# Optimization experiments

Measured on AMD Instinct MI355X. Metric: run time of the kernel, lower is better.

## Reference

```python
import jax, jax.numpy as jnp
import numpy as np

B, C, L, M, EMB, HID = 32, 64, 8192, 32, 256, 64

def setup_inputs() -> dict:
    key = jax.random.key(0)
    ks = jax.random.split(key, 14)
    s_w = 1.0 / (C * C)
    s_a = 1.0 / EMB
    return {
        "x": jax.random.normal(ks[0], (B, C, L), jnp.float32),
        "emb": jax.random.normal(ks[1], (B, EMB), jnp.float32),
        "weights_pos": s_w * jax.random.normal(ks[2], (C, C, M, 2), jnp.float32),
        "weights_neg": s_w * jax.random.normal(ks[3], (C, C, M, 2), jnp.float32),
        "A_real_pos": s_a * jax.random.normal(ks[4], (M, EMB), jnp.float32),
        "A_imag_pos": s_a * jax.random.normal(ks[5], (M, EMB), jnp.float32),
        "A_real_neg": s_a * jax.random.normal(ks[6], (M, EMB), jnp.float32),
        "A_imag_neg": s_a * jax.random.normal(ks[7], (M, EMB), jnp.float32),
        "tm_w1": 0.05 * jax.random.normal(ks[8], (HID, EMB), jnp.float32),
        "tm_b1": jnp.zeros((HID,), jnp.float32),
        "tm_w2": 0.05 * jax.random.normal(ks[9], (2 * C, HID), jnp.float32),
        "tm_b2": jnp.zeros((2 * C,), jnp.float32),
        "lin_w": 0.05 * jax.random.normal(ks[10], (C, C), jnp.float32),
        "lin_b": jnp.zeros((C,), jnp.float32),
    }

def reference(x, emb, weights_pos, weights_neg, A_real_pos, A_imag_pos,
              A_real_neg, A_imag_neg, tm_w1, tm_b1, tm_w2, tm_b2, lin_w, lin_b):
    b, c, l = x.shape
    m = weights_pos.shape[2]
    k = l // 2 + 1
    # ---- SpectralConv1d branch ----
    x_ft = jnp.fft.rfft(x, norm="ortho")  # [B,C,K] complex
    wp = weights_pos[..., 0] + 1j * weights_pos[..., 1]  # [Ci,Co,M]
    wn = weights_neg[..., 0] + 1j * weights_neg[..., 1]
    phi_p = (emb @ A_real_pos.T) + 1j * (emb @ A_imag_pos.T)  # [B,M]
    phi_n = (emb @ A_real_neg.T) + 1j * (emb @ A_imag_neg.T)
    out_pos = jnp.einsum("bim,iom->bom", x_ft[:, :, :m], wp) * phi_p[:, None, :]
    out_neg = jnp.einsum("bim,iom->bom", x_ft[:, :, k - m:], wn) * phi_n[:, None, :]
    out_ft = jnp.zeros((b, c, k), dtype=x_ft.dtype)
    out_ft = out_ft.at[:, :, :m].set(out_pos).at[:, :, k - m:].set(out_neg)
    x1 = jnp.fft.irfft(out_ft, n=l, norm="ortho")  # [B,C,L]
    # ---- Conv1DTime branch (FiLM-style) ----
    h = jax.nn.silu(emb @ tm_w1.T + tm_b1)          # [B,HID]
    gb = h @ tm_w2.T + tm_b2                         # [B,2C]
    gamma, beta = gb[:, :c], gb[:, c:]
    xl = jnp.einsum("bcl,oc->bol", x, lin_w) + lin_b[None, :, None]
    x2 = xl * (1.0 + gamma[:, :, None]) + beta[:, :, None]
    return jax.nn.silu(x1 + x2)
```

## Files before the change

kernel.cpp:

```cpp
#include <hip/hip_runtime.h>
#include <math.h>

#define L_ 8192
#define EMB_ 256
#define HID_ 64

typedef __attribute__((ext_vector_type(8))) short bf16x8;
typedef __attribute__((ext_vector_type(4))) float f32x4;
typedef __attribute__((ext_vector_type(4))) int i32x4;

#define OFF_TFB  0
#define OFF_TLB  262144
#define OFF_AFB  524288
#define OFF_XFRP 917504
#define OFF_B2   3014656
#define OFF_PHI  3016704
#define OFF_GB   3020800

__device__ inline int pkbf(float a, float b) {
    int r;
    asm volatile("v_cvt_pk_bf16_f32 %0, %1, %2" : "=v"(r) : "v"(a), "v"(b));
    return r;
}
__device__ inline bf16x8 asbf(i32x4 v) { union { i32x4 i; bf16x8 h; } u; u.i = v; return u.h; }
#define MFMA(A,B,C) __builtin_amdgcn_mfma_f32_16x16x32_bf16((A),(B),(C),0,0,0)

__device__ inline ushort f2bf(float v) {
    unsigned b = __float_as_uint(v);
    return (ushort)((b + 0x7FFFu + ((b >> 16) & 1u)) >> 16);
}
__device__ inline float bf2f(ushort h) { return __uint_as_float(((unsigned)h) << 16); }
__device__ inline float hwsin(float rev) { float r; asm("v_sin_f32 %0, %1" : "=v"(r) : "v"(rev)); return r; }
__device__ inline float hwcos(float rev) { float r; asm("v_cos_f32 %0, %1" : "=v"(r) : "v"(rev)); return r; }

__global__ __launch_bounds__(256) void k_init(ushort* __restrict__ TLB, ushort* __restrict__ TFB,
        const float* __restrict__ emb,
        const float* __restrict__ Arp, const float* __restrict__ Aip,
        const float* __restrict__ Arn, const float* __restrict__ Ain, float* __restrict__ phi,
        const float* __restrict__ w1, const float* __restrict__ b1,
        const float* __restrict__ w2, const float* __restrict__ b2, float* __restrict__ gb) {
    int bid = blockIdx.x;
    if (bid < 4096) {
        int idx = bid * 256 + threadIdx.x;
        int f, l; ushort* dst;
        if (idx < 524288) {
            int u = idx;
            int e = u & 7, lane = (u >> 3) & 63, ct = (u >> 9) & 3, kstep = u >> 11;
            l = kstep * 32 + ((lane >> 4) << 3) + e;
            f = ct * 16 + (lane & 15);
            dst = TLB + u;
        } else {
            int u = idx - 524288;
            int e = u & 7, lane = (u >> 3) & 63, ts = (u >> 9) & 1, lt = u >> 10;
            l = lt * 16 + (lane & 15);
            f = ts * 32 + ((lane >> 4) << 3) + e;
            dst = TFB + u;
        }
        int fr = f & 31; bool sinp = (f & 32) != 0;
        int r = (fr * l) & (L_ - 1);
        float rev = (float)r * (1.0f / (float)L_);
        float v = sinp ? hwsin(rev) : hwcos(rev);
        *dst = f2bf(v);
    } else if (bid < 4112) {
        int tid = (bid - 4096) * 256 + threadIdx.x;
        int b = tid >> 7;
        int mm = (tid >> 2) & 31;
        int cmp = tid & 3;
        const float* A = (cmp == 0) ? Arp : (cmp == 1) ? Aip : (cmp == 2) ? Arn : Ain;
        const float4* e4 = (const float4*)(emb + b * EMB_);
        const float4* a4 = (const float4*)(A + mm * EMB_);
        float acc = 0.f;
        for (int q = 0; q < EMB_ / 4; ++q) {
            float4 ev = e4[q], av = a4[q];
            acc += ev.x * av.x + ev.y * av.y + ev.z * av.z + ev.w * av.w;
        }
        phi[tid] = acc;
    } else {
        __shared__ float h[HID_];
        int b = bid - 4112, t = threadIdx.x;
        if (t < HID_) {
            const float4* e4 = (const float4*)(emb + b * EMB_);
            const float4* w4 = (const float4*)(w1 + t * EMB_);
            float acc = b1[t];
            for (int q = 0; q < EMB_ / 4; ++q) {
                float4 ev = e4[q], wv = w4[q];
                acc += ev.x * wv.x + ev.y * wv.y + ev.z * wv.z + ev.w * wv.w;
            }
            h[t] = acc / (1.f + expf(-acc));
        }
        __syncthreads();
        if (t < 128) {
            float g = b2[t];
            const float4* h4 = (const float4*)h;
            const float4* w4 = (const float4*)(w2 + t * HID_);
            for (int q = 0; q < HID_ / 4; ++q) {
                float4 hv = h4[q], wv = w4[q];
                g += hv.x * wv.x + hv.y * wv.y + hv.z * wv.z + hv.w * wv.w;
            }
            if (t < 64) gb[(b * 64 + t) * 2 + 0] = 1.f + g;
            else        gb[(b * 64 + (t - 64)) * 2 + 1] = g;
        }
    }
}

__global__ __launch_bounds__(256) void k_dft(const float* __restrict__ x,
        const ushort* __restrict__ TLB, float* __restrict__ xfrp) {
    __shared__ float sP[4][16][132];
    int stripe = blockIdx.x >> 3;
    int lseg = blockIdx.x & 7;
    int w = threadIdx.x >> 6;
    int lane = threadIdx.x & 63;
    int row = lane & 15, koff = (lane >> 4) << 3;
    int r0 = stripe * 16;
    int kb0 = lseg * 1024 + w * 256;

    f32x4 acc[8];
    #pragma unroll
    for (int i = 0; i < 8; ++i) acc[i] = (f32x4){0.f, 0.f, 0.f, 0.f};

    const float* ap = x + (size_t)(r0 + row) * L_ + kb0 + koff;
    const i32x4* tb = (const i32x4*)TLB;
    int tbase = (kb0 >> 5) * 256 + lane;
    const i32x4 SM = {(int)0x80000000, (int)0x80000000, (int)0x80000000, (int)0x80000000};

    float4 xa0 = *(const float4*)(ap);
    float4 xc0 = *(const float4*)(ap + 4);
    float4 xa1 = *(const float4*)(ap + 32);
    float4 xc1 = *(const float4*)(ap + 36);
    float4 xa2 = *(const float4*)(ap + 64);
    float4 xc2 = *(const float4*)(ap + 68);
    i32x4 t0 = tb[tbase], t1 = tb[tbase + 64], t2 = tb[tbase + 128], t3 = tb[tbase + 192];
    #pragma unroll
    for (int ks = 0; ks < 8; ++ks) {
        float4 nxa = {0,0,0,0}, nxc = {0,0,0,0};
        i32x4 n0 = t0, n1 = t1, n2 = t2, n3 = t3;
        if (ks < 5) {
            nxa = *(const float4*)(ap + (ks + 3) * 32);
            nxc = *(const float4*)(ap + (ks + 3) * 32 + 4);
        }
        if (ks < 7) {
            int ti = tbase + (ks + 1) * 256;
            n0 = tb[ti]; n1 = tb[ti + 64]; n2 = tb[ti + 128]; n3 = tb[ti + 192];
        }
        int h0 = pkbf(xa0.x, xa0.y), h1 = pkbf(xa0.z, xa0.w);
        int h2 = pkbf(xc0.x, xc0.y), h3 = pkbf(xc0.z, xc0.w);
        bf16x8 AH = asbf((i32x4){h0, h1, h2, h3});
        acc[0] = MFMA(AH, asbf(t0), acc[0]); acc[4] = MFMA(AH, asbf(t0 ^ SM), acc[4]);
        acc[1] = MFMA(AH, asbf(t1), acc[1]); acc[5] = MFMA(AH, asbf(t1 ^ SM), acc[5]);
        acc[2] = MFMA(AH, asbf(t2), acc[2]); acc[6] = MFMA(AH, asbf(t2 ^ SM), acc[6]);
        acc[3] = MFMA(AH, asbf(t3), acc[3]); acc[7] = MFMA(AH, asbf(t3 ^ SM), acc[7]);
        xa0 = xa1; xc0 = xc1; xa1 = xa2; xc1 = xc2; xa2 = nxa; xc2 = nxc;
        t0 = n0; t1 = n1; t2 = n2; t3 = n3;
    }
    int crow = (lane >> 4) << 2;
    int ccol = lane & 15;
    #pragma unroll
    for (int ct = 0; ct < 8; ++ct)
        #pragma unroll
        for (int r = 0; r < 4; ++r)
            sP[w][crow + r][ct * 16 + ccol] = acc[ct][r];
    __syncthreads();
    #pragma unroll
    for (int i = 0; i < 8; ++i) {
        int e = threadIdx.x + 256 * i;
        int rr = e & 15, cc = e >> 4;
        float s = sP[0][rr][cc] + sP[1][rr][cc] + sP[2][rr][cc] + sP[3][rr][cc];
        xfrp[((size_t)(lseg * 128 + cc)) * 2048 + r0 + rr] = s;
    }
}

__global__ __launch_bounds__(256) void k_mix(const float* __restrict__ xfrt,
        const float* __restrict__ wpos, const float* __restrict__ wneg,
        const float* __restrict__ phi, const float* __restrict__ lw,
        const float* __restrict__ lb, const float* __restrict__ gb,
        ushort* __restrict__ afb, float* __restrict__ bias2) {
    int bi = blockIdx.x;
    int tid = threadIdx.x;
    if (bi >= 256) {
        int b = bi - 256;
        ushort* dst = afb + (size_t)b * 24576;
        #pragma unroll
        for (int j = 0; j < 16; ++j) {
            int u = tid + 256 * j;
            int e = u & 7, lane = (u >> 3) & 63, mt = (u >> 9) & 3, ks2 = u >> 11;
            int c = mt * 16 + (lane & 15);
            int kk = ((lane >> 4) << 3) + e;
            float v = lw[c * 64 + ks2 * 32 + kk] * gb[(b * 64 + c) * 2];
            ushort hi = f2bf(v);
            int base = (((4 + ks2) * 4 + mt) * 64 + lane) * 16;
            dst[base + e] = hi;
            dst[base + 8 + e] = f2bf(v - bf2f(hi));
        }
        if (tid < 64) {
            float g1 = gb[(b * 64 + tid) * 2], be = gb[(b * 64 + tid) * 2 + 1];
            bias2[b * 64 + tid] = lb[tid] * g1 + be;
        }
        return;
    }
    __shared__ float sW[64][64][2];
    __shared__ float sXr[8][64], sXi[8][64];
    int bh = bi & 3, side = (bi >> 2) & 1, mm = bi >> 3;
    int slot = side ? (31 - mm) : mm;
    int colR = side ? (64 + slot) : mm;
    int colI = side ? (96 + slot) : (32 + mm);

    const float* W = side ? wneg : wpos;
    #pragma unroll
    for (int j = 0; j < 16; ++j) {
        int fidx = tid + 256 * j;
        int i = fidx >> 6, o = fidx & 63;
        float2 wv = *(const float2*)&W[(size_t)(i * 64 + o) * 64 + mm * 2];
        sW[i][o][0] = wv.x;
        sW[i][o][1] = wv.y;
    }
    {
        const float2* pR = (const float2*)(xfrt + (size_t)colR * 2048 + bh * 512);
        const float2* pI = (const float2*)(xfrt + (size_t)colI * 2048 + bh * 512);
        float2 aR = {0, 0}, aI = {0, 0};
        #pragma unroll
        for (int s = 0; s < 8; ++s) {
            float2 vR = pR[(size_t)s * 131072 + tid];
            float2 vI = pI[(size_t)s * 131072 + tid];
            aR.x += vR.x; aR.y += vR.y;
            aI.x += vI.x; aI.y += vI.y;
        }
        if (!side) { aI.x = -aI.x; aI.y = -aI.y; }
        *(float2*)&sXr[tid >> 5][(tid & 31) * 2] = aR;
        *(float2*)&sXi[tid >> 5][(tid & 31) * 2] = aI;
    }
    __syncthreads();

    int o = tid & 63, bg = tid >> 6;
    const float invL = 1.f / (float)L_;
    float fac = (slot == 0) ? invL : 2.f * invL;
    int comp = side ? 2 : 0;
    int e = slot & 7, kgrp = slot >> 3;
    int mt = o >> 4, lane = kgrp * 16 + (o & 15);
    #pragma unroll
    for (int bl = 0; bl < 2; ++bl) {
        int b_local = bg * 2 + bl;
        int b = bh * 8 + b_local;
        float sre = 0.f, sim = 0.f;
        #pragma unroll 16
        for (int i = 0; i < 64; ++i) {
            float wr = sW[i][o][0], wi = sW[i][o][1];
            float xr = sXr[b_local][i], xi = sXi[b_local][i];
            sre += xr * wr - xi * wi;
            sim += xr * wi + xi * wr;
        }
        const float* ph = &phi[(b * 32 + mm) * 4 + (side ? 2 : 0)];
        float phr = ph[0], phim = ph[1];
        float Pre = sre * phr - sim * phim;
        float Pim = sre * phim + sim * phr;
        float a = fac * Pre;
        float bcoef = (slot == 0) ? 0.f : (side ? 2.f * invL * Pim : -2.f * invL * Pim);
        ushort* dst = afb + (size_t)b * 24576;
        ushort hiA = f2bf(a);
        int baseA = ((comp * 4 + mt) * 64 + lane) * 16;
        dst[baseA + e] = hiA;
        dst[baseA + 8 + e] = f2bf(a - bf2f(hiA));
        ushort hiB = f2bf(bcoef);
        int baseB = (((comp + 1) * 4 + mt) * 64 + lane) * 16;
        dst[baseB + e] = hiB;
        dst[baseB + 8 + e] = f2bf(bcoef - bf2f(hiB));
    }
}

#define XISSUE(ts, xv)                                                                   \
    _Pragma("unroll")                                                                    \
    for (int nj = 0; nj < 2; ++nj) {                                                     \
        const float* xp = x + (size_t)(b * 64 + (ts) * 32 + kgrp * 8) * L_               \
                            + lbase + nj * 16 + col;                                     \
        _Pragma("unroll")                                                                \
        for (int e = 0; e < 8; ++e) xv[nj][e] = xp[(size_t)e * L_];                      \
    }

#define TPART(ts)                                                                        \
    {                                                                                    \
        i32x4 bh_[2];                                                                    \
        _Pragma("unroll")                                                                \
        for (int nj = 0; nj < 2; ++nj)                                                   \
            bh_[nj] = tb[((lt0 + nj) * 2 + (ts)) * 64 + lane];                           \
        _Pragma("unroll")                                                                \
        for (int mt = 0; mt < 4; ++mt) {                                                 \
            i32x4 ah0 = ab[(((ts) * 4 + mt) * 64 + lane) * 2];                           \
            i32x4 ah1 = ab[(((2 + (ts)) * 4 + mt) * 64 + lane) * 2];                     \
            bf16x8 AH0 = asbf(ah0), AH1 = asbf(ah1);                                     \
            _Pragma("unroll")                                                            \
            for (int nj = 0; nj < 2; ++nj) {                                             \
                acc[mt][nj] = MFMA(AH0, asbf(bh_[nj]), acc[mt][nj]);                     \
                acc[mt][nj] = MFMA(AH1, asbf(bh_[nj] ^ SM), acc[mt][nj]);                \
            }                                                                            \
        }                                                                                \
    }

#define XPART(ts, xv)                                                                    \
    _Pragma("unroll")                                                                    \
    for (int nj = 0; nj < 2; ++nj) {                                                     \
        int h0 = pkbf(xv[nj][0], xv[nj][1]), h1 = pkbf(xv[nj][2], xv[nj][3]);            \
        int h2 = pkbf(xv[nj][4], xv[nj][5]), h3 = pkbf(xv[nj][6], xv[nj][7]);            \
        bf16x8 XH = asbf((i32x4){h0, h1, h2, h3});                                       \
        _Pragma("unroll")                                                                \
        for (int mt = 0; mt < 4; ++mt) {                                                 \
            i32x4 ah = ab[(((4 + (ts)) * 4 + mt) * 64 + lane) * 2];                      \
            acc[mt][nj] = MFMA(asbf(ah), XH, acc[mt][nj]);                               \
        }                                                                                \
    }

__global__ __launch_bounds__(256, 3) void k_fuse(const float* __restrict__ x,
        const ushort* __restrict__ TFB, const ushort* __restrict__ AFB,
        const float* __restrict__ bias2, float* __restrict__ out) {
    int b = blockIdx.x >> 6, lt = blockIdx.x & 63;
    int w = threadIdx.x >> 6, lane = threadIdx.x & 63;
    int col = lane & 15, kgrp = lane >> 4;
    int lbase = lt * 128 + w * 32;
    int lt0 = lbase >> 4;
    const i32x4* tb = (const i32x4*)TFB;
    const i32x4* ab = (const i32x4*)AFB + (size_t)b * 3072;

    f32x4 acc[4][2];
    #pragma unroll
    for (int i = 0; i < 4; ++i)
        #pragma unroll
        for (int j = 0; j < 2; ++j) acc[i][j] = (f32x4){0.f, 0.f, 0.f, 0.f};

    int sm = (col & 1) ? (int)0x80008000 : 0;
    i32x4 SM = {sm, sm, sm, sm};

    float xva[2][8], xvb[2][8];
    XISSUE(0, xva)
    XISSUE(1, xvb)
    TPART(0)
    XPART(0, xva)
    TPART(1)
    XPART(1, xvb)

    #pragma unroll
    for (int mt = 0; mt < 4; ++mt) {
        #pragma unroll
        for (int r = 0; r < 4; ++r) {
            int c = mt * 16 + kgrp * 4 + r;
            float bias = bias2[b * 64 + c];
            float* op = out + (size_t)(b * 64 + c) * L_ + lbase + col;
            #pragma unroll
            for (int nj = 0; nj < 2; ++nj) {
                float v = acc[mt][nj][r] + bias;
                op[nj * 16] = v / (1.f + __expf(-v));
            }
        }
    }
}

extern "C" void kernel_launch(void* const* d_in, const int* in_sizes, int n_in,
                              void* d_out, int out_size, void* d_ws, size_t ws_size,
                              hipStream_t stream) {
    const float* x    = (const float*)d_in[0];
    const float* emb  = (const float*)d_in[1];
    const float* wpos = (const float*)d_in[2];
    const float* wneg = (const float*)d_in[3];
    const float* Arp  = (const float*)d_in[4];
    const float* Aip  = (const float*)d_in[5];
    const float* Arn  = (const float*)d_in[6];
    const float* Ain  = (const float*)d_in[7];
    const float* w1   = (const float*)d_in[8];
    const float* b1   = (const float*)d_in[9];
    const float* w2   = (const float*)d_in[10];
    const float* b2   = (const float*)d_in[11];
    const float* lw   = (const float*)d_in[12];
    const float* lb   = (const float*)d_in[13];
    float* out = (float*)d_out;
    float* ws = (float*)d_ws;
    ushort* TFB  = (ushort*)(ws + OFF_TFB);
    ushort* TLB  = (ushort*)(ws + OFF_TLB);
    ushort* AFB  = (ushort*)(ws + OFF_AFB);
    float*  XFRP = ws + OFF_XFRP;
    float*  B2   = ws + OFF_B2;
    float*  PHI  = ws + OFF_PHI;
    float*  GB   = ws + OFF_GB;

    hipLaunchKernelGGL(k_init,  dim3(4144), dim3(256), 0, stream,
                       TLB, TFB, emb, Arp, Aip, Arn, Ain, PHI, w1, b1, w2, b2, GB);
    hipLaunchKernelGGL(k_dft,   dim3(1024), dim3(256), 0, stream, x, TLB, XFRP);
    hipLaunchKernelGGL(k_mix,   dim3(288),  dim3(256), 0, stream, XFRP, wpos, wneg, PHI,
                       lw, lb, GB, AFB, B2);
    hipLaunchKernelGGL(k_fuse,  dim3(2048), dim3(256), 0, stream, x, TFB, AFB, B2, out);
}
```

Measured before the change: 69.11 us.

## Emit bf16 transposed x from DFT kernel and pre-transpose spectral weights

The DFT kernel now writes the bf16-packed x values into a channel-interleaved workspace buffer. The fused output kernel reads these with a few 16-byte vector loads instead of 16 strided fp32 loads and reconverting them to bf16. The spectral weights are also transposed once in the init kernel, so the mixing kernel can load them with contiguous float4 reads. This trades extra global writes (scattered 2-byte stores in k_dft) and extra workspace for cheaper, coalesced reads downstream.

```diff
diff --git a/kernel.cpp b/kernel.cpp
--- a/kernel.cpp
+++ b/kernel.cpp
@@ -16,6 +16,8 @@
 #define OFF_B2   3014656
 #define OFF_PHI  3016704
 #define OFF_GB   3020800
+#define OFF_WT   3024896
+#define OFF_XT   3549184
 
 __device__ inline int pkbf(float a, float b) {
     int r;
@@ -38,7 +40,8 @@
         const float* __restrict__ Arp, const float* __restrict__ Aip,
         const float* __restrict__ Arn, const float* __restrict__ Ain, float* __restrict__ phi,
         const float* __restrict__ w1, const float* __restrict__ b1,
-        const float* __restrict__ w2, const float* __restrict__ b2, float* __restrict__ gb) {
+        const float* __restrict__ w2, const float* __restrict__ b2, float* __restrict__ gb,
+        const float* __restrict__ wpos, const float* __restrict__ wneg, float* __restrict__ WT) {
     int bid = blockIdx.x;
     if (bid < 4096) {
         int idx = bid * 256 + threadIdx.x;
@@ -75,7 +78,7 @@
             acc += ev.x * av.x + ev.y * av.y + ev.z * av.z + ev.w * av.w;
         }
         phi[tid] = acc;
-    } else {
+    } else if (bid < 4144) {
         __shared__ float h[HID_];
         int b = bid - 4112, t = threadIdx.x;
         if (t < HID_) {
@@ -100,11 +103,24 @@
             if (t < 64) gb[(b * 64 + t) * 2 + 0] = 1.f + g;
             else        gb[(b * 64 + (t - 64)) * 2 + 1] = g;
         }
+    } else {
+        int t = bid - 4144;
+        int side = t >> 6, i = t & 63;
+        const float* W = side ? wneg : wpos;
+        const float* src = W + (size_t)i * 4096;
+        int tid = threadIdx.x;
+        #pragma unroll
+        for (int j = 0; j < 8; ++j) {
+            int u = tid + 256 * j;
+            int mm = u >> 6, o = u & 63;
+            float2 v = *(const float2*)(src + o * 64 + mm * 2);
+            *(float2*)(WT + ((size_t)(side * 32 + mm)) * 8192 + i * 128 + o * 2) = v;
+        }
     }
 }
 
 __global__ __launch_bounds__(256) void k_dft(const float* __restrict__ x,
-        const ushort* __restrict__ TLB, float* __restrict__ xfrp) {
+        const ushort* __restrict__ TLB, float* __restrict__ xfrp, ushort* __restrict__ XT) {
     __shared__ float sP[4][16][132];
     int stripe = blockIdx.x >> 3;
     int lseg = blockIdx.x & 7;
@@ -145,6 +161,13 @@
         int h0 = pkbf(xa0.x, xa0.y), h1 = pkbf(xa0.z, xa0.w);
         int h2 = pkbf(xc0.x, xc0.y), h3 = pkbf(xc0.z, xc0.w);
         bf16x8 AH = asbf((i32x4){h0, h1, h2, h3});
+        {
+            ushort* xtp = XT + (((size_t)stripe * 8192 + kb0 + koff + ks * 32) << 4) + row;
+            xtp[0]   = (ushort)h0;  xtp[16]  = (ushort)((unsigned)h0 >> 16);
+            xtp[32]  = (ushort)h1;  xtp[48]  = (ushort)((unsigned)h1 >> 16);
+            xtp[64]  = (ushort)h2;  xtp[80]  = (ushort)((unsigned)h2 >> 16);
+            xtp[96]  = (ushort)h3;  xtp[112] = (ushort)((unsigned)h3 >> 16);
+        }
         acc[0] = MFMA(AH, asbf(t0), acc[0]); acc[4] = MFMA(AH, asbf(t0 ^ SM), acc[4]);
         acc[1] = MFMA(AH, asbf(t1), acc[1]); acc[5] = MFMA(AH, asbf(t1 ^ SM), acc[5]);
         acc[2] = MFMA(AH, asbf(t2), acc[2]); acc[6] = MFMA(AH, asbf(t2 ^ SM), acc[6]);
@@ -170,7 +193,7 @@
 }
 
 __global__ __launch_bounds__(256) void k_mix(const float* __restrict__ xfrt,
-        const float* __restrict__ wpos, const float* __restrict__ wneg,
+        const float* __restrict__ WT,
         const float* __restrict__ phi, const float* __restrict__ lw,
         const float* __restrict__ lb, const float* __restrict__ gb,
         ushort* __restrict__ afb, float* __restrict__ bias2) {
@@ -204,14 +227,14 @@
     int colR = side ? (64 + slot) : mm;
     int colI = side ? (96 + slot) : (32 + mm);
 
-    const float* W = side ? wneg : wpos;
-    #pragma unroll
-    for (int j = 0; j < 16; ++j) {
-        int fidx = tid + 256 * j;
-        int i = fidx >> 6, o = fidx & 63;
-        float2 wv = *(const float2*)&W[(size_t)(i * 64 + o) * 64 + mm * 2];
-        sW[i][o][0] = wv.x;
-        sW[i][o][1] = wv.y;
+    {
+        const float4* wt = (const float4*)(WT + ((size_t)(side * 32 + mm)) * 8192);
+        float* sWlin = &sW[0][0][0];
+        #pragma unroll
+        for (int j = 0; j < 8; ++j) {
+            int u = tid + 256 * j;
+            *(float4*)&sWlin[u * 4] = wt[u];
+        }
     }
     {
         const float2* pR = (const float2*)(xfrt + (size_t)colR * 2048 + bh * 512);
@@ -265,15 +288,6 @@
         dst[baseB + 8 + e] = f2bf(bcoef - bf2f(hiB));
     }
 }
-
-#define XISSUE(ts, xv)                                                                   \
-    _Pragma("unroll")                                                                    \
-    for (int nj = 0; nj < 2; ++nj) {                                                     \
-        const float* xp = x + (size_t)(b * 64 + (ts) * 32 + kgrp * 8) * L_               \
-                            + lbase + nj * 16 + col;                                     \
-        _Pragma("unroll")                                                                \
-        for (int e = 0; e < 8; ++e) xv[nj][e] = xp[(size_t)e * L_];                      \
-    }
 
 #define TPART(ts)                                                                        \
     {                                                                                    \
@@ -294,20 +308,19 @@
         }                                                                                \
     }
 
-#define XPART(ts, xv)                                                                    \
-    _Pragma("unroll")                                                                    \
-    for (int nj = 0; nj < 2; ++nj) {                                                     \
-        int h0 = pkbf(xv[nj][0], xv[nj][1]), h1 = pkbf(xv[nj][2], xv[nj][3]);            \
-        int h2 = pkbf(xv[nj][4], xv[nj][5]), h3 = pkbf(xv[nj][6], xv[nj][7]);            \
-        bf16x8 XH = asbf((i32x4){h0, h1, h2, h3});                                       \
+#define XPART(ts, xv0, xv1)                                                              \
+    {                                                                                    \
+        bf16x8 XH0 = asbf(xv0), XH1 = asbf(xv1);                                         \
         _Pragma("unroll")                                                                \
         for (int mt = 0; mt < 4; ++mt) {                                                 \
             i32x4 ah = ab[(((4 + (ts)) * 4 + mt) * 64 + lane) * 2];                      \
-            acc[mt][nj] = MFMA(asbf(ah), XH, acc[mt][nj]);                               \
+            bf16x8 AH = asbf(ah);                                                        \
+            acc[mt][0] = MFMA(AH, XH0, acc[mt][0]);                                      \
+            acc[mt][1] = MFMA(AH, XH1, acc[mt][1]);                                      \
         }                                                                                \
     }
 
-__global__ __launch_bounds__(256, 3) void k_fuse(const float* __restrict__ x,
+__global__ __launch_bounds__(256, 3) void k_fuse(const ushort* __restrict__ XT,
         const ushort* __restrict__ TFB, const ushort* __restrict__ AFB,
         const float* __restrict__ bias2, float* __restrict__ out) {
     int b = blockIdx.x >> 6, lt = blockIdx.x & 63;
@@ -317,6 +330,7 @@
     int lt0 = lbase >> 4;
     const i32x4* tb = (const i32x4*)TFB;
     const i32x4* ab = (const i32x4*)AFB + (size_t)b * 3072;
+    const i32x4* xt = (const i32x4*)XT;
 
     f32x4 acc[4][2];
     #pragma unroll
@@ -327,13 +341,17 @@
     int sm = (col & 1) ? (int)0x80008000 : 0;
     i32x4 SM = {sm, sm, sm, sm};
 
-    float xva[2][8], xvb[2][8];
-    XISSUE(0, xva)
-    XISSUE(1, xvb)
+    size_t xs0 = ((size_t)(b * 4 + (kgrp >> 1)) * 8192 + lbase + col) * 2 + (kgrp & 1);
+    size_t xs1 = ((size_t)(b * 4 + 2 + (kgrp >> 1)) * 8192 + lbase + col) * 2 + (kgrp & 1);
+    i32x4 xv00 = xt[xs0];
+    i32x4 xv01 = xt[xs0 + 32];
+    i32x4 xv10 = xt[xs1];
+    i32x4 xv11 = xt[xs1 + 32];
+
     TPART(0)
-    XPART(0, xva)
+    XPART(0, xv00, xv01)
     TPART(1)
-    XPART(1, xvb)
+    XPART(1, xv10, xv11)
 
     #pragma unroll
     for (int mt = 0; mt < 4; ++mt) {
@@ -377,11 +395,14 @@
     float*  B2   = ws + OFF_B2;
     float*  PHI  = ws + OFF_PHI;
     float*  GB   = ws + OFF_GB;
-
-    hipLaunchKernelGGL(k_init,  dim3(4144), dim3(256), 0, stream,
-                       TLB, TFB, emb, Arp, Aip, Arn, Ain, PHI, w1, b1, w2, b2, GB);
-    hipLaunchKernelGGL(k_dft,   dim3(1024), dim3(256), 0, stream, x, TLB, XFRP);
-    hipLaunchKernelGGL(k_mix,   dim3(288),  dim3(256), 0, stream, XFRP, wpos, wneg, PHI,
+    float*  WT   = ws + OFF_WT;
+    ushort* XT   = (ushort*)(ws + OFF_XT);
+
+    hipLaunchKernelGGL(k_init,  dim3(4272), dim3(256), 0, stream,
+                       TLB, TFB, emb, Arp, Aip, Arn, Ain, PHI, w1, b1, w2, b2, GB,
+                       wpos, wneg, WT);
+    hipLaunchKernelGGL(k_dft,   dim3(1024), dim3(256), 0, stream, x, TLB, XFRP, XT);
+    hipLaunchKernelGGL(k_mix,   dim3(288),  dim3(256), 0, stream, XFRP, WT, PHI,
                        lw, lb, GB, AFB, B2);
-    hipLaunchKernelGGL(k_fuse,  dim3(2048), dim3(256), 0, stream, x, TFB, AFB, B2, out);
-}
+    hipLaunchKernelGGL(k_fuse,  dim3(2048), dim3(256), 0, stream, XT, TFB, AFB, B2, out);
+}
```

New measurement: 67.51 us. 1.02x faster.
